# Kernel optimization log

Hardware: AMD Instinct MI355X
Metric: run time of the kernel (lower is better)

The kernel has to match this reference:

```python
import jax, jax.numpy as jnp
import numpy as np

EPS = 1e-5
NUM_HEADS = 4


def _layer_norm(x, g, b):
    m = jnp.mean(x, axis=-1, keepdims=True)
    v = jnp.mean((x - m) ** 2, axis=-1, keepdims=True)
    return (x - m) / jnp.sqrt(v + EPS) * g + b


def setup_inputs() -> dict:
    key = jax.random.key(0)
    ks = jax.random.split(key, 32)
    B, N, ND, TD, L = 100000, 20, 128, 64, 2
    HD = 128  # num_heads * attention_dim
    CD = ND + TD  # 192
    s = 0.02
    inp = {
        "node_features": jax.random.normal(ks[0], (B, ND), jnp.float32),
        "neighbor_features": jax.random.normal(ks[1], (B, N, ND), jnp.float32),
        "node_times": jax.random.uniform(ks[2], (B,), jnp.float32),
        "neighbor_times": jax.random.uniform(ks[3], (B, N), jnp.float32),
        "time_freq": jax.random.normal(ks[4], (TD,), jnp.float32),
        "time_phase": jnp.zeros((TD,), jnp.float32),
        "Wq": jax.random.normal(ks[5], (L, CD, HD), jnp.float32) * s,
        "bq": jnp.zeros((L, HD), jnp.float32),
        "Wk": jax.random.normal(ks[6], (L, CD, HD), jnp.float32) * s,
        "bk": jnp.zeros((L, HD), jnp.float32),
        "Wv": jax.random.normal(ks[7], (L, CD, HD), jnp.float32) * s,
        "bv": jnp.zeros((L, HD), jnp.float32),
        "Wo": jax.random.normal(ks[8], (L, HD, ND), jnp.float32) * s,
        "bo": jnp.zeros((L, ND), jnp.float32),
        "W1": jax.random.normal(ks[9], (L, ND, 2 * ND), jnp.float32) * s,
        "b1": jnp.zeros((L, 2 * ND), jnp.float32),
        "W2": jax.random.normal(ks[10], (L, 2 * ND, ND), jnp.float32) * s,
        "b2": jnp.zeros((L, ND), jnp.float32),
        "g1": jnp.ones((L, ND), jnp.float32),
        "be1": jnp.zeros((L, ND), jnp.float32),
        "g2": jnp.ones((L, ND), jnp.float32),
        "be2": jnp.zeros((L, ND), jnp.float32),
        "Wc1": jax.random.normal(ks[11], (ND, ND // 2), jnp.float32) * s,
        "bc1": jnp.zeros((ND // 2,), jnp.float32),
        "Wc2": jax.random.normal(ks[12], (ND // 2, 1), jnp.float32) * s,
        "bc2": jnp.zeros((1,), jnp.float32),
        "mask": jax.random.randint(ks[13], (B, N), 0, 2, jnp.int32),
    }
    return inp


def reference(node_features, neighbor_features, node_times, neighbor_times,
              time_freq, time_phase, Wq, bq, Wk, bk, Wv, bv, Wo, bo,
              W1, b1, W2, b2, g1, be1, g2, be2, Wc1, bc1, Wc2, bc2, mask):
    L, _, HD = Wq.shape
    B, N, ND = neighbor_features.shape
    H = NUM_HEADS
    D = HD // H
    scale = 1.0 / np.sqrt(D).astype(np.float32)
    # time encodings (Bochner): cos(t * w + phi)
    tq = jnp.cos(node_times[:, None] * time_freq + time_phase)          # [B, TD]
    tk = jnp.cos(neighbor_times[..., None] * time_freq + time_phase)   # [B, N, TD]
    kcomb = jnp.concatenate([neighbor_features, tk], axis=-1)           # [B, N, CD]
    pad = (mask == 0)[:, None, :]                                       # [B, 1, N]
    x = node_features
    for l in range(L):
        qcomb = jnp.concatenate([x, tq], axis=-1)                       # [B, CD]
        q = (qcomb @ Wq[l] + bq[l]).reshape(B, H, D)
        k = (kcomb @ Wk[l] + bk[l]).reshape(B, N, H, D)
        v = (kcomb @ Wv[l] + bv[l]).reshape(B, N, H, D)
        scores = jnp.einsum('bhd,bnhd->bhn', q, k) * scale              # [B, H, N]
        scores = jnp.where(pad, jnp.float32(-1e9), scores)
        w = jax.nn.softmax(scores, axis=-1)
        a = jnp.einsum('bhn,bnhd->bhd', w, v).reshape(B, HD)
        attn = a @ Wo[l] + bo[l]                                        # [B, ND]
        x = _layer_norm(x + attn, g1[l], be1[l])
        ff = jax.nn.relu(x @ W1[l] + b1[l]) @ W2[l] + b2[l]
        x = _layer_norm(x + ff, g2[l], be2[l])
    h = jax.nn.relu(x @ Wc1 + bc1)
    return jax.nn.sigmoid(h @ Wc2 + bc2)                                # [B, 1]
```

## Files before the change

### kernel.cpp

```cpp
#include <hip/hip_runtime.h>

#define BB 100000
#define NN 20
#define ND 128
#define TD 64
#define CD 192
#define HD 128
#define NH 4
#define DH 32
#define NL 2
#define WLS 311296

typedef __attribute__((ext_vector_type(8))) short bf16x8;
typedef __attribute__((ext_vector_type(4))) float f32x4;

static __device__ __forceinline__ float bf2f(unsigned short u) {
  return __uint_as_float(((unsigned)u) << 16);
}
static __device__ __forceinline__ unsigned short f2bf(float x) {
  unsigned b = __float_as_uint(x);
  return (unsigned short)((b + 0x7FFFu + ((b >> 16) & 1u)) >> 16);
}
static __device__ __forceinline__ bf16x8 load_a8(const float* p) {
  float4 a = *(const float4*)p, b = *(const float4*)(p + 4);
  bf16x8 r;
  r[0] = (short)f2bf(a.x); r[1] = (short)f2bf(a.y);
  r[2] = (short)f2bf(a.z); r[3] = (short)f2bf(a.w);
  r[4] = (short)f2bf(b.x); r[5] = (short)f2bf(b.y);
  r[6] = (short)f2bf(b.z); r[7] = (short)f2bf(b.w);
  return r;
}
static __device__ __forceinline__ int fragidx(int wk, int c16) {
  return (((wk >> 3) << 4) | c16) * 8 + (wk & 7);
}


__global__ __launch_bounds__(192) void precomp_M(
    const float* __restrict__ Wq, const float* __restrict__ Wk,
    unsigned short* __restrict__ WF) {
  int e = blockIdx.x;
  int c1 = e % CD;
  int h = (e / CD) % NH;
  int l = e / (CD * NH);
  int c2 = threadIdx.x;
  const float* wq = Wq + ((size_t)l * CD + c1) * HD + h * DH;
  const float* wk = Wk + ((size_t)l * CD + c2) * HD + h * DH;
  float acc = 0.f;
#pragma unroll
  for (int d = 0; d < DH; ++d) acc += wq[d] * wk[d];
  int n = h * CD + c2;
  int nt = n >> 4, c16 = n & 15;
  int kt = c1 >> 5, wk2 = c1 & 31;
  WF[(size_t)l * WLS + (size_t)(kt * 48 + nt) * 512 + fragidx(wk2, c16)] =
      f2bf(acc);
}

__global__ __launch_bounds__(192) void precomp_pk(
    const float* __restrict__ bq, const float* __restrict__ Wk,
    float* __restrict__ pk) {
  int e = blockIdx.x;
  int h = e % NH, l = e / NH;
  int c2 = threadIdx.x;
  const float* bqp = bq + (size_t)l * HD + h * DH;
  const float* wk = Wk + ((size_t)l * CD + c2) * HD + h * DH;
  float acc = 0.f;
#pragma unroll
  for (int d = 0; d < DH; ++d) acc += bqp[d] * wk[d];
  pk[(size_t)l * 768 + h * CD + c2] = acc;
}

__global__ __launch_bounds__(128) void precomp_WC(
    const float* __restrict__ Wv, const float* __restrict__ Wo,
    unsigned short* __restrict__ WF) {
  int e = blockIdx.x;
  int k = e % 768, l = e / 768;
  int c = k % CD, h = k / CD;
  int j = threadIdx.x;
  const float* wv = Wv + ((size_t)l * CD + c) * HD + h * DH;
  const float* wo = Wo + ((size_t)l * HD + h * DH) * ND + j;
  float acc = 0.f;
#pragma unroll
  for (int d = 0; d < DH; ++d) acc += wv[d] * wo[(size_t)d * ND];
  int kt = k >> 5, wk2 = k & 31;
  int nt = j >> 4, c16 = j & 15;
  WF[(size_t)l * WLS + 147456 + (size_t)(kt * 8 + nt) * 512 +
     fragidx(wk2, c16)] = f2bf(acc);
}

__global__ __launch_bounds__(128) void precomp_bC(
    const float* __restrict__ bv, const float* __restrict__ bo,
    const float* __restrict__ Wo, float* __restrict__ bC) {
  int l = blockIdx.x;
  int j = threadIdx.x;
  float acc = bo[(size_t)l * ND + j];
  for (int k = 0; k < HD; ++k)
    acc += bv[(size_t)l * HD + k] * Wo[((size_t)l * HD + k) * ND + j];
  bC[(size_t)l * ND + j] = acc;
}

__global__ __launch_bounds__(256) void conv_w2(
    const float* __restrict__ W1, const float* __restrict__ W2,
    unsigned short* __restrict__ WF) {
  int t = blockIdx.x;
  int l = t >> 7, tt = t & 127;
#pragma unroll
  for (int e = 0; e < 2; ++e) {
    int idx = threadIdx.x * 2 + e;
    int lane = idx >> 3, j = idx & 7;
    int wk = ((lane >> 4) << 3) + j;
    int c16 = lane & 15;
    float v;
    size_t dst;
    if (tt < 64) {
      int kt = tt >> 4, n2 = tt & 15;
      v = W1[((size_t)l * ND + kt * 32 + wk) * (2 * ND) + n2 * 16 + c16];
      dst = (size_t)l * WLS + 245760 + (size_t)tt * 512 + idx;
    } else {
      int t2 = tt - 64;
      int kt = t2 >> 3, n2 = t2 & 7;
      v = W2[((size_t)l * 2 * ND + kt * 32 + wk) * ND + n2 * 16 + c16];
      dst = (size_t)l * WLS + 278528 + (size_t)t2 * 512 + idx;
    }
    WF[dst] = f2bf(v);
  }
}

__global__ __launch_bounds__(256) void prep_tq(
    const float* __restrict__ ntime, const float* __restrict__ tf,
    const float* __restrict__ tp, float* __restrict__ tqf) {
  int i = blockIdx.x * 256 + threadIdx.x;
  int b = i >> 6, j = i & 63;
  tqf[i] = __cosf(ntime[b] * tf[j] + tp[j]);
}

__global__ __launch_bounds__(256) void prep_mb(const int* __restrict__ mask,
                                               unsigned* __restrict__ mb) {
  int e = blockIdx.x * 256 + threadIdx.x;
  if (e < BB) {
    unsigned m = 0;
    for (int n = 0; n < NN; ++n)
      m |= (mask[(size_t)e * NN + n] != 0 ? 1u : 0u) << n;
    mb[e] = m;
  }
}

template <int TN, int ABF, int OBF>
__global__ __launch_bounds__(256) void gemm16(
    const void* __restrict__ A, int lda,
    const float* __restrict__ A2, int lda2, int ksplit,
    const unsigned short* __restrict__ BF,
    int ktiles, int ntiles,
    const float* __restrict__ bias,
    void* __restrict__ C, int ldc, int relu) {
  const int tid = threadIdx.x;
  const int wv = tid >> 6, lane = tid & 63;
  const int NW = blockDim.x >> 6;
  const int m0 = blockIdx.x << 4;
  const int arow = m0 + (lane & 15);
  const int kgrp = (lane >> 4) << 3;
  f32x4 acc[TN];
#pragma unroll
  for (int i = 0; i < TN; ++i) acc[i] = f32x4{0.f, 0.f, 0.f, 0.f};
  for (int kt = 0; kt < ktiles; ++kt) {
    bf16x8 af;
    if (kt * 32 >= ksplit) {
      af = load_a8(A2 + (size_t)arow * lda2 + (kt * 32 - ksplit) + kgrp);
    } else if (ABF) {
      af = *(const bf16x8*)((const unsigned short*)A + (size_t)arow * lda +
                            kt * 32 + kgrp);
    } else {
      af = load_a8((const float*)A + (size_t)arow * lda + kt * 32 + kgrp);
    }
#pragma unroll
    for (int i = 0; i < TN; ++i) {
      int nt = wv + NW * i;
      bf16x8 bf = *(const bf16x8*)(BF + (((size_t)(kt * ntiles + nt)) << 9) +
                                   (lane << 3));
      acc[i] = __builtin_amdgcn_mfma_f32_16x16x32_bf16(af, bf, acc[i], 0, 0, 0);
    }
  }
  const int crow = m0 + ((lane >> 4) << 2);
#pragma unroll
  for (int i = 0; i < TN; ++i) {
    int nt = wv + NW * i;
    int col = nt * 16 + (lane & 15);
    float bv = bias ? bias[col] : 0.f;
#pragma unroll
    for (int rr = 0; rr < 4; ++rr) {
      float v = acc[i][rr] + bv;
      if (relu) v = fmaxf(v, 0.f);
      if (OBF)
        ((unsigned short*)C)[(size_t)(crow + rr) * ldc + col] = f2bf(v);
      else
        ((float*)C)[(size_t)(crow + rr) * ldc + col] = v;
    }
  }
}

template <int ABF, int CLS>
__global__ __launch_bounds__(256) void gemm_ln(
    const void* __restrict__ A, int lda, int ktiles,
    const unsigned short* __restrict__ BF,
    const float* __restrict__ bias, const float* __restrict__ res,
    const float* __restrict__ gamma, const float* __restrict__ beta,
    float* __restrict__ xout,
    const float* __restrict__ Wc1, const float* __restrict__ bc1,
    const float* __restrict__ Wc2, const float* __restrict__ bc2,
    float* __restrict__ out) {
  __shared__ float Cs[16][132];
  __shared__ float hsh[16][64];
  const int tid = threadIdx.x;
  const int wv = tid >> 6, lane = tid & 63;
  const int m0 = blockIdx.x << 4;
  const int arow = m0 + (lane & 15);
  const int kgrp = (lane >> 4) << 3;
  const int nt0 = wv, nt1 = wv + 4;
  f32x4 acc0 = {0.f, 0.f, 0.f, 0.f}, acc1 = {0.f, 0.f, 0.f, 0.f};
  for (int kt = 0; kt < ktiles; ++kt) {
    bf16x8 af;
    if (ABF)
      af = *(const bf16x8*)((const unsigned short*)A + (size_t)arow * lda +
                            kt * 32 + kgrp);
    else
      af = load_a8((const float*)A + (size_t)arow * lda + kt * 32 + kgrp);
    bf16x8 b0 = *(const bf16x8*)(BF + (((size_t)(kt * 8 + nt0)) << 9) + (lane << 3));
    bf16x8 b1 = *(const bf16x8*)(BF + (((size_t)(kt * 8 + nt1)) << 9) + (lane << 3));
    acc0 = __builtin_amdgcn_mfma_f32_16x16x32_bf16(af, b0, acc0, 0, 0, 0);
    acc1 = __builtin_amdgcn_mfma_f32_16x16x32_bf16(af, b1, acc1, 0, 0, 0);
  }
  {
    const int lrow = (lane >> 4) << 2;
    int c0 = nt0 * 16 + (lane & 15), c1 = nt1 * 16 + (lane & 15);
    float bv0 = bias[c0], bv1 = bias[c1];
#pragma unroll
    for (int rr = 0; rr < 4; ++rr) {
      Cs[lrow + rr][c0] = acc0[rr] + bv0;
      Cs[lrow + rr][c1] = acc1[rr] + bv1;
    }
  }
  __syncthreads();
#pragma unroll
  for (int rr = 0; rr < 4; ++rr) {
    int rw = wv * 4 + rr;
    size_t grow = (size_t)(m0 + rw) * ND;
    float y0 = Cs[rw][lane] + res[grow + lane];
    float y1 = Cs[rw][lane + 64] + res[grow + lane + 64];
    float s = y0 + y1, ss = y0 * y0 + y1 * y1;
#pragma unroll
    for (int off = 32; off > 0; off >>= 1) {
      s += __shfl_xor(s, off);
      ss += __shfl_xor(ss, off);
    }
    float mean = s * (1.f / ND);
    float var = ss * (1.f / ND) - mean * mean;
    float rstd = rsqrtf(var + 1e-5f);
    float x0 = (y0 - mean) * rstd * gamma[lane] + beta[lane];
    float x1 = (y1 - mean) * rstd * gamma[lane + 64] + beta[lane + 64];
    if (CLS) {
      Cs[rw][lane] = x0;
      Cs[rw][lane + 64] = x1;
    } else {
      xout[grow + lane] = x0;
      xout[grow + lane + 64] = x1;
    }
  }
  if (CLS) {
    __syncthreads();
#pragma unroll
    for (int rep = 0; rep < 4; ++rep) {
      int idx = rep * 256 + tid;
      int row = idx >> 6, j = idx & 63;
      float acc = 0.f;
      for (int c = 0; c < ND; ++c) acc += Cs[row][c] * Wc1[c * 64 + j];
      hsh[row][j] = fmaxf(acc + bc1[j], 0.f);
    }
    __syncthreads();
#pragma unroll
    for (int rr = 0; rr < 4; ++rr) {
      int row = wv * 4 + rr;
      float p = hsh[row][lane] * Wc2[lane];
#pragma unroll
      for (int off = 32; off > 0; off >>= 1) p += __shfl_xor(p, off);
      if (lane == 0)
        out[m0 + row] = 1.f / (1.f + expf(-(p + bc2[0])));
    }
  }
}

__global__ __launch_bounds__(256) void attn_b(
    const float* __restrict__ nbf, const float* __restrict__ nbt,
    const float* __restrict__ tf, const float* __restrict__ tp,
    const unsigned* __restrict__ mb, const unsigned short* __restrict__ r,
    unsigned short* __restrict__ u) {
  __shared__ __align__(16) unsigned short kcb[2][NN][200];
  __shared__ __align__(16) float rs[2][768];
  __shared__ __align__(16) float scs[2][NH][NN];
  __shared__ unsigned msks[2];
  const int tid = threadIdx.x;
  const size_t e0 = (size_t)blockIdx.x * 2;

  if (tid < 192) {
    uint4 v = *(const uint4*)(r + e0 * 768 + tid * 8);
    const unsigned short* pv = (const unsigned short*)&v;
    float* dst = &rs[0][0] + tid * 8;
#pragma unroll
    for (int k = 0; k < 8; ++k) dst[k] = bf2f(pv[k]);
  }
  for (int i = tid; i < 2 * NN * 32; i += 256) {
    int el = i / (NN * 32), rem = i % (NN * 32);
    int n = rem >> 5, cq = rem & 31;
    float4 v = *(const float4*)&nbf[((e0 + el) * NN + n) * ND + cq * 4];
    ushort4 o;
    o.x = f2bf(v.x); o.y = f2bf(v.y); o.z = f2bf(v.z); o.w = f2bf(v.w);
    *(ushort4*)&kcb[el][n][cq * 4] = o;
  }
  for (int i = tid; i < 2 * NN * 32; i += 256) {
    int el = i / (NN * 32), rem = i % (NN * 32);
    int n = rem >> 5, jp = (rem & 31) * 2;
    float t = nbt[(e0 + el) * NN + n];
    unsigned a = f2bf(__cosf(t * tf[jp] + tp[jp]));
    unsigned b = f2bf(__cosf(t * tf[jp + 1] + tp[jp + 1]));
    *(unsigned*)&kcb[el][n][ND + jp] = a | (b << 16);
  }
  if (tid < 2) msks[tid] = mb[e0 + tid];
  __syncthreads();
  if (tid < 2 * NH * NN) {
    int el = tid / (NH * NN), rem = tid % (NH * NN);
    int h = rem / NN, n = rem % NN;
    const float* rp = &rs[el][h * CD];
    const unsigned short* kp = &kcb[el][n][0];
    float acc = 0.f;
    for (int c = 0; c < CD; c += 4) {
      float4 rv = *(const float4*)&rp[c];
      ushort4 kv = *(const ushort4*)&kp[c];
      acc += rv.x * bf2f(kv.x) + rv.y * bf2f(kv.y) + rv.z * bf2f(kv.z) +
             rv.w * bf2f(kv.w);
    }
    scs[el][h][n] =
        ((msks[el] >> n) & 1u) ? acc * 0.17677669529663687f : -1e9f;
  }
  __syncthreads();
  if (tid < 2 * NH) {
    int el = tid >> 2, h = tid & 3;
    float mx = -3.4e38f;
#pragma unroll
    for (int n = 0; n < NN; ++n) mx = fmaxf(mx, scs[el][h][n]);
    float ev[NN], s = 0.f;
#pragma unroll
    for (int n = 0; n < NN; ++n) { ev[n] = __expf(scs[el][h][n] - mx); s += ev[n]; }
    float inv = 1.f / s;
#pragma unroll
    for (int n = 0; n < NN; ++n) scs[el][h][n] = ev[n] * inv;
  }
  __syncthreads();
  for (int i = tid; i < 2 * NH * (CD / 4); i += 256) {
    int el = i / (NH * 48), rem = i % (NH * 48);
    int h = rem / 48, cq = (rem % 48) * 4;
    float a0 = 0.f, a1 = 0.f, a2 = 0.f, a3 = 0.f;
#pragma unroll
    for (int n = 0; n < NN; ++n) {
      float w = scs[el][h][n];
      ushort4 kv = *(const ushort4*)&kcb[el][n][cq];
      a0 += w * bf2f(kv.x); a1 += w * bf2f(kv.y);
      a2 += w * bf2f(kv.z); a3 += w * bf2f(kv.w);
    }
    ushort4 o;
    o.x = f2bf(a0); o.y = f2bf(a1); o.z = f2bf(a2); o.w = f2bf(a3);
    *(ushort4*)&u[(e0 + el) * 768 + h * CD + cq] = o;
  }
}

#define G 2
#define T 256
#define KCS 196
#define RUS 772

__global__ __launch_bounds__(T, 4) void tgat_fused(
    const float* __restrict__ nf, const float* __restrict__ nbf,
    const float* __restrict__ nt, const float* __restrict__ nbt,
    const float* __restrict__ tf, const float* __restrict__ tp,
    const float* __restrict__ Wq, const float* __restrict__ bq,
    const float* __restrict__ Wk,
    const float* __restrict__ Wv, const float* __restrict__ bv,
    const float* __restrict__ Wo, const float* __restrict__ bo,
    const float* __restrict__ W1, const float* __restrict__ b1,
    const float* __restrict__ W2, const float* __restrict__ b2,
    const float* __restrict__ g1, const float* __restrict__ be1,
    const float* __restrict__ g2, const float* __restrict__ be2,
    const float* __restrict__ Wc1, const float* __restrict__ bc1,
    const float* __restrict__ Wc2, const float* __restrict__ bc2,
    const int* __restrict__ mask,
    float* __restrict__ out) {
  __shared__ __align__(16) unsigned short kc[G][NN][KCS];
  __shared__ __align__(16) float xs[G][ND];
  __shared__ __align__(16) float tqs[G][TD];
  __shared__ __align__(16) float ys[G][HD];
  __shared__ __align__(16) float rus[G][RUS];
  __shared__ __align__(16) float scs[G][NH][NN];
  __shared__ __align__(16) float h1s[G][2 * ND];
  __shared__ __align__(16) unsigned msks[G];
  float* asv = &h1s[0][0];
  const int tid = threadIdx.x;
  const int b0 = blockIdx.x * G;
  {
    int g = tid >> 7, j = tid & 127;
    xs[g][j] = nf[(b0 + g) * ND + j];
  }
  if (tid < G * TD) {
    int g = tid >> 6, j = tid & 63;
    tqs[g][j] = __cosf(nt[b0 + g] * tf[j] + tp[j]);
  }
  if (tid < G) {
    unsigned m = 0;
    for (int n = 0; n < NN; ++n)
      m |= (mask[(b0 + tid) * NN + n] != 0 ? 1u : 0u) << n;
    msks[tid] = m;
  }
  for (int idx = tid; idx < G * NN * (ND / 4); idx += T) {
    int g = idx / (NN * 32), rem = idx % (NN * 32);
    int n = rem >> 5, cq = rem & 31;
    float4 v = *(const float4*)&nbf[(((b0 + g) * NN + n) * ND) + cq * 4];
    ushort4 o;
    o.x = f2bf(v.x); o.y = f2bf(v.y); o.z = f2bf(v.z); o.w = f2bf(v.w);
    *(ushort4*)&kc[g][n][cq * 4] = o;
  }
  for (int idx = tid; idx < G * NN * TD; idx += T) {
    int g = idx / (NN * TD), rem = idx % (NN * TD);
    int n = rem >> 6, j = rem & 63;
    kc[g][n][ND + j] = f2bf(__cosf(nbt[(b0 + g) * NN + n] * tf[j] + tp[j]));
  }
  __syncthreads();
  const float scale = 0.17677669529663687f;
  for (int l = 0; l < NL; ++l) {
    {
      int g = tid >> 7, j = tid & 127;
      const float* wq = Wq + (l * CD) * HD + j;
      float acc = bq[l * HD + j];
      for (int c = 0; c < CD; c += 4) {
        float4 qv = (c < ND) ? *(const float4*)&xs[g][c]
                             : *(const float4*)&tqs[g][c - ND];
        acc += qv.x * wq[(c + 0) * HD] + qv.y * wq[(c + 1) * HD] +
               qv.z * wq[(c + 2) * HD] + qv.w * wq[(c + 3) * HD];
      }
      ys[g][j] = acc;
    }
    __syncthreads();
    for (int rep = 0; rep < 3; ++rep) {
      int i = rep * T + tid;
      int h = i / CD;
      int c2 = i - h * CD;
      const float* wk = Wk + (l * CD + c2) * HD + h * DH;
      const float* yp0 = &ys[0][h * DH];
      const float* yp1 = &ys[1][h * DH];
      float a0 = 0.f, a1 = 0.f;
#pragma unroll
      for (int d = 0; d < DH; d += 4) {
        float4 w4 = *(const float4*)&wk[d];
        float4 y0 = *(const float4*)&yp0[d];
        float4 y1 = *(const float4*)&yp1[d];
        a0 += y0.x * w4.x + y0.y * w4.y + y0.z * w4.z + y0.w * w4.w;
        a1 += y1.x * w4.x + y1.y * w4.y + y1.z * w4.z + y1.w * w4.w;
      }
      rus[0][i] = a0;
      rus[1][i] = a1;
    }
    __syncthreads();
    if (tid < G * NH * NN) {
      int g = tid / (NH * NN), rem = tid % (NH * NN);
      int h = rem / NN, n = rem % NN;
      const float* rp = &rus[g][h * CD];
      const unsigned short* kp = &kc[g][n][0];
      float acc = 0.f;
      for (int c = 0; c < CD; c += 4) {
        float4 rv = *(const float4*)&rp[c];
        ushort4 kv = *(const ushort4*)&kp[c];
        acc += rv.x * bf2f(kv.x) + rv.y * bf2f(kv.y) + rv.z * bf2f(kv.z) +
               rv.w * bf2f(kv.w);
      }
      scs[g][h][n] = ((msks[g] >> n) & 1u) ? acc * scale : -1e9f;
    }
    __syncthreads();
    if (tid < G * NH) {
      int g = tid / NH, h = tid % NH;
      float mx = -3.4e38f;
#pragma unroll
      for (int n = 0; n < NN; ++n) mx = fmaxf(mx, scs[g][h][n]);
      float ev[NN], s = 0.f;
#pragma unroll
      for (int n = 0; n < NN; ++n) { ev[n] = __expf(scs[g][h][n] - mx); s += ev[n]; }
      float inv = 1.f / s;
#pragma unroll
      for (int n = 0; n < NN; ++n) scs[g][h][n] = ev[n] * inv;
    }
    __syncthreads();
    for (int flat = tid; flat < G * NH * (CD / 4); flat += T) {
      int g = flat / (NH * 48), iq = flat % (NH * 48);
      int h = iq / 48, c = (iq % 48) * 4;
      const unsigned short* kp = &kc[g][0][0];
      float a0 = 0.f, a1 = 0.f, a2 = 0.f, a3 = 0.f;
#pragma unroll
      for (int n = 0; n < NN; ++n) {
        float w = scs[g][h][n];
        ushort4 kv = *(const ushort4*)&kp[n * KCS + c];
        a0 += w * bf2f(kv.x); a1 += w * bf2f(kv.y);
        a2 += w * bf2f(kv.z); a3 += w * bf2f(kv.w);
      }
      *(float4*)&rus[g][h * CD + c] = make_float4(a0, a1, a2, a3);
    }
    __syncthreads();
    {
      int j = tid & (HD - 1);
      int g = tid >> 7;
      int h = j >> 5;
      const float* wv = Wv + (l * CD) * HD + j;
      float acc = 0.f;
      for (int c = 0; c < CD; c += 4) {
        float4 uv = *(const float4*)&rus[g][h * CD + c];
        acc += uv.x * wv[(c + 0) * HD] + uv.y * wv[(c + 1) * HD] +
               uv.z * wv[(c + 2) * HD] + uv.w * wv[(c + 3) * HD];
      }
      asv[g * HD + j] = acc + bv[l * HD + j];
    }
    __syncthreads();
    {
      int j = tid & (ND - 1);
      int g = tid >> 7;
      const float* wo = Wo + (l * HD) * ND + j;
      float acc = 0.f;
      for (int c = 0; c < HD; c += 4) {
        float4 av = *(const float4*)&asv[g * HD + c];
        acc += av.x * wo[(c + 0) * ND] + av.y * wo[(c + 1) * ND] +
               av.z * wo[(c + 2) * ND] + av.w * wo[(c + 3) * ND];
      }
      rus[g][j] = acc + bo[l * ND + j];
    }
    __syncthreads();
    if (tid < G * 64) {
      int g = tid >> 6, lane = tid & 63;
      float y0 = xs[g][lane] + rus[g][lane];
      float y1 = xs[g][lane + 64] + rus[g][lane + 64];
      float s = y0 + y1, ss = y0 * y0 + y1 * y1;
#pragma unroll
      for (int off = 32; off > 0; off >>= 1) {
        s += __shfl_xor(s, off);
        ss += __shfl_xor(ss, off);
      }
      float mean = s * (1.f / ND);
      float var = ss * (1.f / ND) - mean * mean;
      float rstd = rsqrtf(var + 1e-5f);
      xs[g][lane] = (y0 - mean) * rstd * g1[l * ND + lane] + be1[l * ND + lane];
      xs[g][lane + 64] =
          (y1 - mean) * rstd * g1[l * ND + lane + 64] + be1[l * ND + lane + 64];
    }
    __syncthreads();
    {
      int j = tid;
      const float* w1p = W1 + (l * ND) * (2 * ND) + j;
      float acc0 = 0.f, acc1 = 0.f;
      for (int c = 0; c < ND; c += 4) {
        float w0 = w1p[(c + 0) * 2 * ND], wa = w1p[(c + 1) * 2 * ND],
              w2 = w1p[(c + 2) * 2 * ND], w3 = w1p[(c + 3) * 2 * ND];
        float4 x0 = *(const float4*)&xs[0][c];
        float4 x1 = *(const float4*)&xs[1][c];
        acc0 += x0.x * w0 + x0.y * wa + x0.z * w2 + x0.w * w3;
        acc1 += x1.x * w0 + x1.y * wa + x1.z * w2 + x1.w * w3;
      }
      float b1v = b1[l * 2 * ND + j];
      h1s[0][j] = fmaxf(acc0 + b1v, 0.f);
      h1s[1][j] = fmaxf(acc1 + b1v, 0.f);
    }
    __syncthreads();
    {
      int j = tid & (ND - 1);
      int g = tid >> 7;
      const float* w2p = W2 + (l * 2 * ND) * ND + j;
      float acc = 0.f;
      for (int c = 0; c < 2 * ND; c += 4) {
        float4 hv = *(const float4*)&h1s[g][c];
        acc += hv.x * w2p[(c + 0) * ND] + hv.y * w2p[(c + 1) * ND] +
               hv.z * w2p[(c + 2) * ND] + hv.w * w2p[(c + 3) * ND];
      }
      rus[g][j] = acc + b2[l * ND + j];
    }
    __syncthreads();
    if (tid < G * 64) {
      int g = tid >> 6, lane = tid & 63;
      float y0 = xs[g][lane] + rus[g][lane];
      float y1 = xs[g][lane + 64] + rus[g][lane + 64];
      float s = y0 + y1, ss = y0 * y0 + y1 * y1;
#pragma unroll
      for (int off = 32; off > 0; off >>= 1) {
        s += __shfl_xor(s, off);
        ss += __shfl_xor(ss, off);
      }
      float mean = s * (1.f / ND);
      float var = ss * (1.f / ND) - mean * mean;
      float rstd = rsqrtf(var + 1e-5f);
      xs[g][lane] = (y0 - mean) * rstd * g2[l * ND + lane] + be2[l * ND + lane];
      xs[g][lane + 64] =
          (y1 - mean) * rstd * g2[l * ND + lane + 64] + be2[l * ND + lane + 64];
    }
    __syncthreads();
  }
  if (tid < G * 64) {
    int j = tid & 63;
    int g = tid >> 6;
    const float* wc = Wc1 + j;
    float acc = 0.f;
    for (int c = 0; c < ND; c += 4) {
      float4 xv = *(const float4*)&xs[g][c];
      acc += xv.x * wc[(c + 0) * 64] + xv.y * wc[(c + 1) * 64] +
             xv.z * wc[(c + 2) * 64] + xv.w * wc[(c + 3) * 64];
    }
    ((float*)scs)[g * 64 + j] = fmaxf(acc + bc1[j], 0.f);
  }
  __syncthreads();
  if (tid < G * 64) {
    int g = tid >> 6, lane = tid & 63;
    float p = ((float*)scs)[g * 64 + lane] * Wc2[lane];
#pragma unroll
    for (int off = 32; off > 0; off >>= 1) p += __shfl_xor(p, off);
    if (lane == 0) {
      float z = p + bc2[0];
      out[b0 + g] = 1.f / (1.f + expf(-z));
    }
  }
}

extern "C" void kernel_launch(void* const* d_in, const int* in_sizes, int n_in,
                              void* d_out, int out_size, void* d_ws,
                              size_t ws_size, hipStream_t stream) {
  (void)in_sizes; (void)n_in; (void)out_size;
  const float* nf  = (const float*)d_in[0];
  const float* nbf = (const float*)d_in[1];
  const float* ntm = (const float*)d_in[2];
  const float* nbt = (const float*)d_in[3];
  const float* tf  = (const float*)d_in[4];
  const float* tp  = (const float*)d_in[5];
  const float* Wq  = (const float*)d_in[6];
  const float* bq  = (const float*)d_in[7];
  const float* Wk  = (const float*)d_in[8];
  const float* Wv  = (const float*)d_in[10];
  const float* bv  = (const float*)d_in[11];
  const float* Wo  = (const float*)d_in[12];
  const float* bo  = (const float*)d_in[13];
  const float* W1  = (const float*)d_in[14];
  const float* b1  = (const float*)d_in[15];
  const float* W2  = (const float*)d_in[16];
  const float* b2  = (const float*)d_in[17];
  const float* g1  = (const float*)d_in[18];
  const float* be1 = (const float*)d_in[19];
  const float* g2  = (const float*)d_in[20];
  const float* be2 = (const float*)d_in[21];
  const float* Wc1 = (const float*)d_in[22];
  const float* bc1 = (const float*)d_in[23];
  const float* Wc2 = (const float*)d_in[24];
  const float* bc2 = (const float*)d_in[25];
  const int* mask  = (const int*)d_in[26];
  float* out = (float*)d_out;

  const size_t NEED = 283252352ull;
  if (ws_size >= NEED) {
    char* w = (char*)d_ws;
    unsigned short* WF = (unsigned short*)w;
    float* pk = (float*)(w + 1245184);
    float* bC = (float*)(w + 1251328);
    unsigned* mb = (unsigned*)(w + 1252352);
    float* tqf = (float*)(w + 1652352);
    unsigned short* rb = (unsigned short*)(w + 27252352);
    unsigned short* h1b = (unsigned short*)(w + 180852352);
    float* xfb = (float*)(w + 232052352);

    precomp_M<<<NL * NH * CD, CD, 0, stream>>>(Wq, Wk, WF);
    precomp_pk<<<NL * NH, CD, 0, stream>>>(bq, Wk, pk);
    precomp_WC<<<NL * 768, ND, 0, stream>>>(Wv, Wo, WF);
    precomp_bC<<<NL, ND, 0, stream>>>(bv, bo, Wo, bC);
    conv_w2<<<256, 256, 0, stream>>>(W1, W2, WF);
    prep_tq<<<25000, 256, 0, stream>>>(ntm, tf, tp, tqf);
    prep_mb<<<(BB + 255) / 256, 256, 0, stream>>>(mask, mb);

    const float* xsrc = nf;
    for (int l = 0; l < NL; ++l) {
      const unsigned short* WFl = WF + (size_t)l * WLS;
      gemm16<12, 0, 1><<<6250, 256, 0, stream>>>(
          xsrc, ND, tqf, TD, 128, WFl, 6, 48, pk + l * 768, rb, 768, 0);
      attn_b<<<50000, 256, 0, stream>>>(nbf, nbt, tf, tp, mb, rb, rb);
      gemm_ln<1, 0><<<6250, 256, 0, stream>>>(
          rb, 768, 24, WFl + 147456, bC + l * ND, xsrc, g1 + l * ND,
          be1 + l * ND, xfb, nullptr, nullptr, nullptr, nullptr, nullptr);
      gemm16<4, 0, 1><<<6250, 256, 0, stream>>>(
          xfb, ND, nullptr, 0, 1 << 30, WFl + 245760, 4, 16,
          b1 + l * 2 * ND, h1b, 2 * ND, 1);
      if (l == NL - 1)
        gemm_ln<1, 1><<<6250, 256, 0, stream>>>(
            h1b, 2 * ND, 8, WFl + 278528, b2 + l * ND, xfb, g2 + l * ND,
            be2 + l * ND, xfb, Wc1, bc1, Wc2, bc2, out);
      else
        gemm_ln<1, 0><<<6250, 256, 0, stream>>>(
            h1b, 2 * ND, 8, WFl + 278528, b2 + l * ND, xfb, g2 + l * ND,
            be2 + l * ND, xfb, nullptr, nullptr, nullptr, nullptr, nullptr);
      xsrc = xfb;
    }
  } else {
    tgat_fused<<<BB / G, T, 0, stream>>>(nf, nbf, ntm, nbt, tf, tp, Wq, bq, Wk,
                                         Wv, bv, Wo, bo, W1, b1, W2, b2, g1,
                                         be1, g2, be2, Wc1, bc1, Wc2, bc2,
                                         mask, out);
  }
}
```

Baseline: 1.565 ms.

## Tile GEMMs over 64 rows per block to reuse weight fragments

Replaces the 16-row-per-block projection GEMM and GEMM+LayerNorm kernels with 512-thread kernels that each cover 64 rows (four 16-row MFMA tiles). Each weight fragment loaded per wave is reused across the four row tiles, which cuts redundant weight loads from global/L2. The number of blocks drops fourfold and rows past the batch size are clamped or masked. The cost is more accumulator registers per thread and larger shared buffers, which may lower occupancy.

```diff
diff --git a/kernel.cpp b/kernel.cpp
--- a/kernel.cpp
+++ b/kernel.cpp
@@ -144,10 +144,60 @@
   }
 }
 
+__global__ __launch_bounds__(512) void gemm_rt(
+    const float* __restrict__ A, const float* __restrict__ A2,
+    const unsigned short* __restrict__ BF, const float* __restrict__ pk,
+    unsigned short* __restrict__ C) {
+  const int tid = threadIdx.x;
+  const int wv = tid >> 6, lane = tid & 63;
+  const int m0 = blockIdx.x << 6;
+  const int kgrp = (lane >> 4) << 3;
+  f32x4 acc[4][6];
+#pragma unroll
+  for (int rt = 0; rt < 4; ++rt)
+#pragma unroll
+    for (int i = 0; i < 6; ++i) acc[rt][i] = f32x4{0.f, 0.f, 0.f, 0.f};
+#pragma unroll
+  for (int kt = 0; kt < 6; ++kt) {
+    bf16x8 bfr[6];
+#pragma unroll
+    for (int i = 0; i < 6; ++i)
+      bfr[i] = *(const bf16x8*)(BF + (((size_t)(kt * 48 + wv * 6 + i)) << 9) +
+                                (lane << 3));
+#pragma unroll
+    for (int rt = 0; rt < 4; ++rt) {
+      int ar = m0 + rt * 16 + (lane & 15);
+      if (ar > BB - 1) ar = BB - 1;
+      bf16x8 af;
+      if (kt < 4)
+        af = load_a8(A + (size_t)ar * ND + kt * 32 + kgrp);
+      else
+        af = load_a8(A2 + (size_t)ar * TD + (kt - 4) * 32 + kgrp);
+#pragma unroll
+      for (int i = 0; i < 6; ++i)
+        acc[rt][i] = __builtin_amdgcn_mfma_f32_16x16x32_bf16(af, bfr[i],
+                                                             acc[rt][i], 0, 0, 0);
+    }
+  }
+#pragma unroll
+  for (int rt = 0; rt < 4; ++rt) {
+    int crow = m0 + rt * 16 + ((lane >> 4) << 2);
+#pragma unroll
+    for (int i = 0; i < 6; ++i) {
+      int col = (wv * 6 + i) * 16 + (lane & 15);
+      float bv = pk[col];
+#pragma unroll
+      for (int rr = 0; rr < 4; ++rr) {
+        if (crow + rr < BB)
+          C[(size_t)(crow + rr) * 768 + col] = f2bf(acc[rt][i][rr] + bv);
+      }
+    }
+  }
+}
+
 template <int TN, int ABF, int OBF>
 __global__ __launch_bounds__(256) void gemm16(
     const void* __restrict__ A, int lda,
-    const float* __restrict__ A2, int lda2, int ksplit,
     const unsigned short* __restrict__ BF,
     int ktiles, int ntiles,
     const float* __restrict__ bias,
@@ -163,14 +213,11 @@
   for (int i = 0; i < TN; ++i) acc[i] = f32x4{0.f, 0.f, 0.f, 0.f};
   for (int kt = 0; kt < ktiles; ++kt) {
     bf16x8 af;
-    if (kt * 32 >= ksplit) {
-      af = load_a8(A2 + (size_t)arow * lda2 + (kt * 32 - ksplit) + kgrp);
-    } else if (ABF) {
+    if (ABF)
       af = *(const bf16x8*)((const unsigned short*)A + (size_t)arow * lda +
                             kt * 32 + kgrp);
-    } else {
+    else
       af = load_a8((const float*)A + (size_t)arow * lda + kt * 32 + kgrp);
-    }
 #pragma unroll
     for (int i = 0; i < TN; ++i) {
       int nt = wv + NW * i;
@@ -197,9 +244,9 @@
   }
 }
 
-template <int ABF, int CLS>
-__global__ __launch_bounds__(256) void gemm_ln(
-    const void* __restrict__ A, int lda, int ktiles,
+template <int KT, int CLS>
+__global__ __launch_bounds__(512) void gemm_ln_rt(
+    const unsigned short* __restrict__ A, int lda,
     const unsigned short* __restrict__ BF,
     const float* __restrict__ bias, const float* __restrict__ res,
     const float* __restrict__ gamma, const float* __restrict__ beta,
@@ -207,81 +254,83 @@
     const float* __restrict__ Wc1, const float* __restrict__ bc1,
     const float* __restrict__ Wc2, const float* __restrict__ bc2,
     float* __restrict__ out) {
-  __shared__ float Cs[16][132];
-  __shared__ float hsh[16][64];
+  __shared__ float Cs[64][132];
+  __shared__ float hsh[CLS ? 64 : 1][64];
   const int tid = threadIdx.x;
   const int wv = tid >> 6, lane = tid & 63;
-  const int m0 = blockIdx.x << 4;
-  const int arow = m0 + (lane & 15);
+  const int m0 = blockIdx.x << 6;
   const int kgrp = (lane >> 4) << 3;
-  const int nt0 = wv, nt1 = wv + 4;
-  f32x4 acc0 = {0.f, 0.f, 0.f, 0.f}, acc1 = {0.f, 0.f, 0.f, 0.f};
-  for (int kt = 0; kt < ktiles; ++kt) {
-    bf16x8 af;
-    if (ABF)
-      af = *(const bf16x8*)((const unsigned short*)A + (size_t)arow * lda +
-                            kt * 32 + kgrp);
-    else
-      af = load_a8((const float*)A + (size_t)arow * lda + kt * 32 + kgrp);
-    bf16x8 b0 = *(const bf16x8*)(BF + (((size_t)(kt * 8 + nt0)) << 9) + (lane << 3));
-    bf16x8 b1 = *(const bf16x8*)(BF + (((size_t)(kt * 8 + nt1)) << 9) + (lane << 3));
-    acc0 = __builtin_amdgcn_mfma_f32_16x16x32_bf16(af, b0, acc0, 0, 0, 0);
-    acc1 = __builtin_amdgcn_mfma_f32_16x16x32_bf16(af, b1, acc1, 0, 0, 0);
+  f32x4 acc[4];
+#pragma unroll
+  for (int rt = 0; rt < 4; ++rt) acc[rt] = f32x4{0.f, 0.f, 0.f, 0.f};
+#pragma unroll
+  for (int kt = 0; kt < KT; ++kt) {
+    bf16x8 bf = *(const bf16x8*)(BF + (((size_t)(kt * 8 + wv)) << 9) +
+                                 (lane << 3));
+#pragma unroll
+    for (int rt = 0; rt < 4; ++rt) {
+      int ar = m0 + rt * 16 + (lane & 15);
+      if (ar > BB - 1) ar = BB - 1;
+      bf16x8 af = *(const bf16x8*)(A + (size_t)ar * lda + kt * 32 + kgrp);
+      acc[rt] = __builtin_amdgcn_mfma_f32_16x16x32_bf16(af, bf, acc[rt], 0, 0, 0);
+    }
   }
   {
-    const int lrow = (lane >> 4) << 2;
-    int c0 = nt0 * 16 + (lane & 15), c1 = nt1 * 16 + (lane & 15);
-    float bv0 = bias[c0], bv1 = bias[c1];
-#pragma unroll
-    for (int rr = 0; rr < 4; ++rr) {
-      Cs[lrow + rr][c0] = acc0[rr] + bv0;
-      Cs[lrow + rr][c1] = acc1[rr] + bv1;
+    int c0 = wv * 16 + (lane & 15);
+    float bv = bias[c0];
+#pragma unroll
+    for (int rt = 0; rt < 4; ++rt) {
+      int lrow = rt * 16 + ((lane >> 4) << 2);
+#pragma unroll
+      for (int rr = 0; rr < 4; ++rr) Cs[lrow + rr][c0] = acc[rt][rr] + bv;
     }
   }
   __syncthreads();
 #pragma unroll
-  for (int rr = 0; rr < 4; ++rr) {
-    int rw = wv * 4 + rr;
-    size_t grow = (size_t)(m0 + rw) * ND;
-    float y0 = Cs[rw][lane] + res[grow + lane];
-    float y1 = Cs[rw][lane + 64] + res[grow + lane + 64];
-    float s = y0 + y1, ss = y0 * y0 + y1 * y1;
-#pragma unroll
-    for (int off = 32; off > 0; off >>= 1) {
-      s += __shfl_xor(s, off);
-      ss += __shfl_xor(ss, off);
-    }
-    float mean = s * (1.f / ND);
-    float var = ss * (1.f / ND) - mean * mean;
-    float rstd = rsqrtf(var + 1e-5f);
-    float x0 = (y0 - mean) * rstd * gamma[lane] + beta[lane];
-    float x1 = (y1 - mean) * rstd * gamma[lane + 64] + beta[lane + 64];
-    if (CLS) {
-      Cs[rw][lane] = x0;
-      Cs[rw][lane + 64] = x1;
-    } else {
-      xout[grow + lane] = x0;
-      xout[grow + lane + 64] = x1;
+  for (int k = 0; k < 8; ++k) {
+    int rw = wv * 8 + k;
+    if (m0 + rw < BB) {
+      size_t grow = (size_t)(m0 + rw) * ND;
+      float y0 = Cs[rw][lane] + res[grow + lane];
+      float y1 = Cs[rw][lane + 64] + res[grow + lane + 64];
+      float s = y0 + y1, ss = y0 * y0 + y1 * y1;
+#pragma unroll
+      for (int off = 32; off > 0; off >>= 1) {
+        s += __shfl_xor(s, off);
+        ss += __shfl_xor(ss, off);
+      }
+      float mean = s * (1.f / ND);
+      float var = ss * (1.f / ND) - mean * mean;
+      float rstd = rsqrtf(var + 1e-5f);
+      float x0 = (y0 - mean) * rstd * gamma[lane] + beta[lane];
+      float x1 = (y1 - mean) * rstd * gamma[lane + 64] + beta[lane + 64];
+      if (CLS) {
+        Cs[rw][lane] = x0;
+        Cs[rw][lane + 64] = x1;
+      } else {
+        xout[grow + lane] = x0;
+        xout[grow + lane + 64] = x1;
+      }
     }
   }
   if (CLS) {
     __syncthreads();
 #pragma unroll
-    for (int rep = 0; rep < 4; ++rep) {
-      int idx = rep * 256 + tid;
+    for (int rep = 0; rep < 8; ++rep) {
+      int idx = rep * 512 + tid;
       int row = idx >> 6, j = idx & 63;
-      float acc = 0.f;
-      for (int c = 0; c < ND; ++c) acc += Cs[row][c] * Wc1[c * 64 + j];
-      hsh[row][j] = fmaxf(acc + bc1[j], 0.f);
-    }
-    __syncthreads();
-#pragma unroll
-    for (int rr = 0; rr < 4; ++rr) {
-      int row = wv * 4 + rr;
+      float a = 0.f;
+      for (int c = 0; c < ND; ++c) a += Cs[row][c] * Wc1[c * 64 + j];
+      hsh[row][j] = fmaxf(a + bc1[j], 0.f);
+    }
+    __syncthreads();
+#pragma unroll
+    for (int k = 0; k < 8; ++k) {
+      int row = wv * 8 + k;
       float p = hsh[row][lane] * Wc2[lane];
 #pragma unroll
       for (int off = 32; off > 0; off >>= 1) p += __shfl_xor(p, off);
-      if (lane == 0)
+      if (lane == 0 && m0 + row < BB)
         out[m0 + row] = 1.f / (1.f + expf(-(p + bc2[0])));
     }
   }
@@ -679,25 +728,24 @@
     prep_tq<<<25000, 256, 0, stream>>>(ntm, tf, tp, tqf);
     prep_mb<<<(BB + 255) / 256, 256, 0, stream>>>(mask, mb);
 
+    const int GRT = (BB + 63) / 64;
     const float* xsrc = nf;
     for (int l = 0; l < NL; ++l) {
       const unsigned short* WFl = WF + (size_t)l * WLS;
-      gemm16<12, 0, 1><<<6250, 256, 0, stream>>>(
-          xsrc, ND, tqf, TD, 128, WFl, 6, 48, pk + l * 768, rb, 768, 0);
+      gemm_rt<<<GRT, 512, 0, stream>>>(xsrc, tqf, WFl, pk + l * 768, rb);
       attn_b<<<50000, 256, 0, stream>>>(nbf, nbt, tf, tp, mb, rb, rb);
-      gemm_ln<1, 0><<<6250, 256, 0, stream>>>(
-          rb, 768, 24, WFl + 147456, bC + l * ND, xsrc, g1 + l * ND,
+      gemm_ln_rt<24, 0><<<GRT, 512, 0, stream>>>(
+          rb, 768, WFl + 147456, bC + l * ND, xsrc, g1 + l * ND,
           be1 + l * ND, xfb, nullptr, nullptr, nullptr, nullptr, nullptr);
       gemm16<4, 0, 1><<<6250, 256, 0, stream>>>(
-          xfb, ND, nullptr, 0, 1 << 30, WFl + 245760, 4, 16,
-          b1 + l * 2 * ND, h1b, 2 * ND, 1);
+          xfb, ND, WFl + 245760, 4, 16, b1 + l * 2 * ND, h1b, 2 * ND, 1);
       if (l == NL - 1)
-        gemm_ln<1, 1><<<6250, 256, 0, stream>>>(
-            h1b, 2 * ND, 8, WFl + 278528, b2 + l * ND, xfb, g2 + l * ND,
+        gemm_ln_rt<8, 1><<<GRT, 512, 0, stream>>>(
+            h1b, 2 * ND, WFl + 278528, b2 + l * ND, xfb, g2 + l * ND,
             be2 + l * ND, xfb, Wc1, bc1, Wc2, bc2, out);
       else
-        gemm_ln<1, 0><<<6250, 256, 0, stream>>>(
-            h1b, 2 * ND, 8, WFl + 278528, b2 + l * ND, xfb, g2 + l * ND,
+        gemm_ln_rt<8, 0><<<GRT, 512, 0, stream>>>(
+            h1b, 2 * ND, WFl + 278528, b2 + l * ND, xfb, g2 + l * ND,
             be2 + l * ND, xfb, nullptr, nullptr, nullptr, nullptr, nullptr);
       xsrc = xfb;
     }
```

New measurement: 1.762 ms. 12.6% more time.
